# Kernel tuning notes

Hardware: AMD Instinct MI355X
Metric: run time of the kernel (lower is better)

Reference implementation:

```python
import math
import jax
import jax.numpy as jnp
import numpy as np
from jax import lax

B_, L, D_MODEL = 2, 1024, 2048
D_STATE, D_CONV, EXPAND = 16, 4, 2
D_INNER = EXPAND * D_MODEL          # 4096
DT_RANK = math.ceil(D_MODEL / 16)   # 128


def setup_inputs() -> dict:
    key = jax.random.key(0)
    ks = jax.random.split(key, 8)
    hidden_states = jax.random.normal(ks[0], (B_, L, D_MODEL), jnp.float32)
    in_proj_w = jax.random.normal(ks[1], (2 * D_INNER, D_MODEL), jnp.float32) * (D_MODEL ** -0.5)
    conv_w = jax.random.normal(ks[2], (D_INNER, D_CONV), jnp.float32) * (D_CONV ** -0.5)
    conv_b = jnp.zeros((D_INNER,), jnp.float32)
    x_proj_w = jax.random.normal(ks[3], (DT_RANK + 2 * D_STATE, D_INNER), jnp.float32) * (D_INNER ** -0.5)
    dt_std = DT_RANK ** -0.5
    dt_proj_w = jax.random.uniform(ks[4], (D_INNER, DT_RANK), jnp.float32, minval=-dt_std, maxval=dt_std)
    # dt bias init: softplus^{-1} of dt sampled log-uniform in [1e-3, 1e-1]
    dt = jnp.exp(jax.random.uniform(ks[5], (D_INNER,), jnp.float32)
                 * (math.log(0.1) - math.log(0.001)) + math.log(0.001))
    dt = jnp.clip(dt, 1e-4)
    dt_proj_b = dt + jnp.log(-jnp.expm1(-dt))
    A_log = jnp.log(jnp.broadcast_to(jnp.arange(1, D_STATE + 1, dtype=jnp.float32), (D_INNER, D_STATE)))
    D = jnp.ones((D_INNER,), jnp.float32)
    out_proj_w = jax.random.normal(ks[6], (D_MODEL, D_INNER), jnp.float32) * (D_INNER ** -0.5)
    return {
        'hidden_states': hidden_states, 'in_proj_w': in_proj_w,
        'conv_w': conv_w, 'conv_b': conv_b, 'x_proj_w': x_proj_w,
        'dt_proj_w': dt_proj_w, 'dt_proj_b': dt_proj_b,
        'A_log': A_log, 'D': D, 'out_proj_w': out_proj_w,
    }


def _silu(v):
    return v * jax.nn.sigmoid(v)


def _mamba_forward(hidden_states, in_proj_w, conv_w, conv_b, x_proj_w,
                   dt_proj_w, dt_proj_b, A_log, D, out_proj_w):
    b, l, _ = hidden_states.shape
    # in_proj: (b,l,d_model) -> (b, 2*d_inner, l)
    xz = jnp.einsum('bld,ed->bel', hidden_states, in_proj_w)
    x, z = xz[:, :D_INNER, :], xz[:, D_INNER:, :]
    A = -jnp.exp(A_log.astype(jnp.float32))  # (d_inner, d_state)
    # causal depthwise conv1d + SiLU
    xp = jnp.pad(x, ((0, 0), (0, 0), (D_CONV - 1, 0)))
    x = lax.conv_general_dilated(
        xp, conv_w[:, None, :], window_strides=(1,), padding='VALID',
        dimension_numbers=('NCH', 'OIH', 'NCH'), feature_group_count=D_INNER)
    x = _silu(x + conv_b[None, :, None])  # (b, d_inner, l)
    # x_proj -> dt, B, C
    x_dbl = jnp.einsum('bdl,kd->blk', x, x_proj_w)  # (b,l,dt_rank+2n)
    dt_lo = x_dbl[..., :DT_RANK]
    Bmat = x_dbl[..., DT_RANK:DT_RANK + D_STATE]          # (b,l,n)
    Cmat = x_dbl[..., DT_RANK + D_STATE:]                 # (b,l,n)
    delta = jax.nn.softplus(jnp.einsum('blr,dr->bld', dt_lo, dt_proj_w)
                            + dt_proj_b.astype(jnp.float32))  # (b,l,d)
    xt = jnp.transpose(x, (2, 0, 1))       # (l,b,d)
    dl = jnp.transpose(delta, (1, 0, 2))   # (l,b,d)
    Bl = jnp.transpose(Bmat, (1, 0, 2))    # (l,b,n)
    Cl = jnp.transpose(Cmat, (1, 0, 2))    # (l,b,n)

    def step(h, inp):
        d_t, B_t, C_t, x_t = inp
        dA = jnp.exp(d_t[..., None] * A)                       # (b,d,n)
        h = h * dA + d_t[..., None] * B_t[:, None, :] * x_t[..., None]
        y_t = jnp.sum(h * C_t[:, None, :], axis=-1)            # (b,d)
        return h, y_t

    h0 = jnp.zeros((b, D_INNER, D_STATE), jnp.float32)
    _, ys = lax.scan(step, h0, (dl, Bl, Cl, xt))  # ys: (l,b,d)
    y = jnp.transpose(ys, (1, 0, 2))              # (b,l,d)
    y = y + jnp.transpose(x, (0, 2, 1)) * D[None, None, :]
    y = y * _silu(jnp.transpose(z, (0, 2, 1)))
    out = jnp.einsum('bld,ed->ble', y, out_proj_w)  # (b,l,d_model)
    return out


def reference(hidden_states, in_proj_w, conv_w, conv_b, x_proj_w,
              dt_proj_w, dt_proj_b, A_log, D, out_proj_w):
    return _mamba_forward(hidden_states, in_proj_w, conv_w, conv_b, x_proj_w,
                          dt_proj_w, dt_proj_b, A_log, D, out_proj_w)
```

## Files before the change

kernel.cpp:

```cpp
#include <hip/hip_runtime.h>
#include <hip/hip_bf16.h>
#include <stdint.h>

#define BB 2
#define LL 1024
#define DMODEL 2048
#define DINNER 4096
#define DSTATE 16
#define DTRANK 128
#define XDBL_LD 256
#define CHUNK 64
#define NCH (LL / CHUNK)

typedef unsigned short ushort;
using short8 = __attribute__((ext_vector_type(8))) short;
using f32x4  = __attribute__((ext_vector_type(4))) float;
using us4    = __attribute__((ext_vector_type(4))) ushort;

__device__ __forceinline__ float bf2f(ushort u) {
    union { uint32_t i; float f; } v; v.i = ((uint32_t)u) << 16; return v.f;
}
__device__ __forceinline__ ushort f2bf(float f) {
    union { float f; uint32_t i; } v; v.f = f;
    uint32_t lsb = (v.i >> 16) & 1u;
    uint32_t r = v.i + 0x7FFFu + lsb;
    return (ushort)(r >> 16);
}

__device__ __forceinline__ void glds16(const ushort* g, ushort* l) {
    __builtin_amdgcn_global_load_lds(
        (const __attribute__((address_space(1))) void*)g,
        (__attribute__((address_space(3))) void*)l,
        16, 0, 0);
}

__global__ __launch_bounds__(256) void cvt_all(
    const float4* __restrict__ hidden, const float4* __restrict__ inproj,
    const float4* __restrict__ dtw, const float4* __restrict__ outp,
    const float4* __restrict__ xproj,
    us4* __restrict__ hid_h, us4* __restrict__ inp_h, us4* __restrict__ dtp_h,
    us4* __restrict__ outp_h, us4* __restrict__ xpp)
{
    long i = (long)blockIdx.x * 256 + threadIdx.x;
    const float4* src; us4* dst; long j;
    if (i < 1048576)      { src = hidden; dst = hid_h;  j = i; }
    else if (i < 5242880) { src = inproj; dst = inp_h;  j = i - 1048576; }
    else if (i < 5373952) { src = dtw;    dst = dtp_h;  j = i - 5242880; }
    else if (i < 7471104) { src = outp;   dst = outp_h; j = i - 5373952; }
    else {
        j = i - 7471104; dst = xpp;
        if (j >= 163840) { us4 z = {0, 0, 0, 0}; dst[j] = z; return; }
        src = xproj;
    }
    float4 v = src[j];
    us4 o; o.x = f2bf(v.x); o.y = f2bf(v.y); o.z = f2bf(v.z); o.w = f2bf(v.w);
    dst[j] = o;
}

template <bool WF, bool WH>
__global__ __launch_bounds__(512, 4) void gemm_bk32(
    const ushort* __restrict__ A, int lda,
    const ushort* __restrict__ Bm, int ldb,
    float* __restrict__ Cf, ushort* __restrict__ Ch, int ldc,
    int K)
{
    __shared__ __align__(16) ushort sA[2][128 * 32];
    __shared__ __align__(16) ushort sB[2][256 * 32];

    const int tid  = threadIdx.x;
    const int lane = tid & 63;
    const int wave = tid >> 6;
    const int wr   = wave >> 2;
    const int wcol = wave & 3;
    const int lrow = lane & 15;
    const int lg   = lane >> 4;
    const int kswz = (lg ^ ((lrow >> 1) & 3)) << 4;

    const int NT = gridDim.x, MT = gridDim.y;
    int mt, nt;
    if ((NT & 7) == 0) {
        int lin   = blockIdx.y * NT + blockIdx.x;
        int strip = NT >> 3;
        int xcd   = lin & 7;
        int idx   = lin >> 3;
        nt = xcd * strip + (idx % strip);
        mt = idx / strip;
    } else { mt = blockIdx.y; nt = blockIdx.x; }
    const long m0 = (long)mt * 128;
    const long n0 = (long)nt * 256;

    const long zoff = (long)blockIdx.z;
    A  += zoff * (long)K;
    Bm += zoff * (long)K;
    const long Mrows = (long)MT * 128;
    if (WF) Cf += zoff * Mrows * (long)ldc;

    f32x4 acc[4][4] = {};

    const int srow = tid >> 2;
    const int scol = (((tid & 3) ^ ((tid >> 3) & 3)) << 3);
    const ushort* Ag = A  + (m0 + srow) * (long)lda + scol;
    const ushort* Bg = Bm + (n0 + srow) * (long)ldb + scol;
    const long bstep = 128 * (long)ldb;

    const int NKT = K >> 5;

    glds16(Ag, &sA[0][0] + tid * 8);
    glds16(Bg, &sB[0][0] + tid * 8);
    glds16(Bg + bstep, &sB[0][0] + (512 + tid) * 8);
    __syncthreads();

    const int arow0 = (wr * 64 + lrow) * 64 + kswz;
    const int brow0 = (wcol * 64 + lrow) * 64 + kswz;

    for (int kt = 0; kt < NKT; ++kt) {
        const int p = kt & 1;
        const char* sap = (const char*)&sA[p][0];
        const char* sbp = (const char*)&sB[p][0];
        ushort* dA = &sA[p ^ 1][0] + tid * 8;
        ushort* dB = &sB[p ^ 1][0] + tid * 8;
        const long kn = (long)(kt + 1) << 5;
        const bool pf = (kt + 1 < NKT);

        short8 af[4], bf[4];
        #pragma unroll
        for (int i = 0; i < 4; ++i)
            af[i] = *(const short8*)(sap + arow0 + (i * 16) * 64);
        #pragma unroll
        for (int j = 0; j < 4; ++j)
            bf[j] = *(const short8*)(sbp + brow0 + (j * 16) * 64);

        if (pf) {
            glds16(Ag + kn, dA);
            glds16(Bg + kn, dB);
            glds16(Bg + bstep + kn, dB + 512 * 8);
        }

        __builtin_amdgcn_s_setprio(1);
        #pragma unroll
        for (int i = 0; i < 4; ++i)
            #pragma unroll
            for (int j = 0; j < 4; ++j)
                acc[i][j] = __builtin_amdgcn_mfma_f32_16x16x32_bf16(
                    af[i], bf[j], acc[i][j], 0, 0, 0);
        __builtin_amdgcn_s_setprio(0);

        __syncthreads();
    }

    const int r0 = (lane >> 4) * 4;
    const int c0 = lane & 15;
    #pragma unroll
    for (int i = 0; i < 4; ++i) {
        #pragma unroll
        for (int j = 0; j < 4; ++j) {
            const long col = n0 + wcol * 64 + j * 16 + c0;
            #pragma unroll
            for (int r = 0; r < 4; ++r) {
                const long row = m0 + wr * 64 + i * 16 + r0 + r;
                const float v = acc[i][j][r];
                const long idx = row * (long)ldc + col;
                if (WF) Cf[idx] = v;
                if (WH) Ch[idx] = f2bf(v);
            }
        }
    }
}

template <bool WF, bool WH>
__global__ __launch_bounds__(512, 2) void gemm_nt256(
    const ushort* __restrict__ A, int lda,
    const ushort* __restrict__ Bm, int ldb,
    float* __restrict__ Cf, ushort* __restrict__ Ch, int ldc,
    int K)
{
    __shared__ __align__(16) ushort sA[2][256 * 64];
    __shared__ __align__(16) ushort sB[2][256 * 64];

    const int tid  = threadIdx.x;
    const int lane = tid & 63;
    const int wave = tid >> 6;
    const int wr   = wave >> 2;
    const int wcol = wave & 3;
    const int lrow = lane & 15;
    const int lg   = lane >> 4;
    const int s7   = lane & 7;
    const int kb0 = ((0 + lg) ^ s7) << 4;
    const int kb1 = ((4 + lg) ^ s7) << 4;

    const int NT = gridDim.x, MT = gridDim.y;
    int mt, nt;
    if ((NT & 7) == 0) {
        int lin   = blockIdx.y * NT + blockIdx.x;
        int strip = NT >> 3;
        int xcd   = lin & 7;
        int idx   = lin >> 3;
        nt = xcd * strip + (idx % strip);
        mt = idx / strip;
    } else { mt = blockIdx.y; nt = blockIdx.x; }
    const long m0 = (long)mt * 256;
    const long n0 = (long)nt * 256;

    const long zoff = (long)blockIdx.z;
    A  += zoff * (long)K;
    Bm += zoff * (long)K;
    const long Mrows = (long)MT * 256;
    if (WF) Cf += zoff * Mrows * (long)ldc;

    f32x4 acc[8][4] = {};

    const int sr   = tid >> 3;
    const int scol = (((tid & 7) ^ (sr & 7)) << 3);
    const ushort* Ag = A  + (m0 + sr) * (long)lda + scol;
    const ushort* Bg = Bm + (n0 + sr) * (long)ldb + scol;

    const int NKT = K >> 6;

    {
        ushort* dA0 = &sA[0][0] + tid * 8;
        ushort* dB0 = &sB[0][0] + tid * 8;
        #pragma unroll
        for (int c = 0; c < 4; ++c) {
            glds16(Ag + (c * 64) * (long)lda, dA0 + c * 4096);
            glds16(Bg + (c * 64) * (long)ldb, dB0 + c * 4096);
        }
    }
    __syncthreads();

    const int arow0 = (wr * 128 + lrow) * 128;
    const int brow0 = (wcol * 64 + lrow) * 128;

    for (int kt = 0; kt < NKT; ++kt) {
        const int p = kt & 1;
        const char* sap = (const char*)&sA[p][0];
        const char* sbp = (const char*)&sB[p][0];
        ushort* dA = &sA[p ^ 1][0] + tid * 8;
        ushort* dB = &sB[p ^ 1][0] + tid * 8;
        const long kn = (long)(kt + 1) << 6;
        const bool pf = (kt + 1 < NKT);

        short8 bf[4][2];
        #pragma unroll
        for (int j = 0; j < 4; ++j) {
            const int bb = brow0 + (j * 16) * 128;
            bf[j][0] = *(const short8*)(sbp + bb + kb0);
            bf[j][1] = *(const short8*)(sbp + bb + kb1);
        }

        #pragma unroll
        for (int mh = 0; mh < 2; ++mh) {
            short8 af[4][2];
            #pragma unroll
            for (int i4 = 0; i4 < 4; ++i4) {
                const int ab = arow0 + (mh * 64 + i4 * 16) * 128;
                af[i4][0] = *(const short8*)(sap + ab + kb0);
                af[i4][1] = *(const short8*)(sap + ab + kb1);
            }
            if (pf) {
                if (mh == 0) {
                    #pragma unroll
                    for (int c = 0; c < 4; ++c)
                        glds16(Ag + (c * 64) * (long)lda + kn, dA + c * 4096);
                } else {
                    #pragma unroll
                    for (int c = 0; c < 4; ++c)
                        glds16(Bg + (c * 64) * (long)ldb + kn, dB + c * 4096);
                }
            }
            __builtin_amdgcn_s_setprio(1);
            #pragma unroll
            for (int ks = 0; ks < 2; ++ks)
                #pragma unroll
                for (int i4 = 0; i4 < 4; ++i4)
                    #pragma unroll
                    for (int j = 0; j < 4; ++j)
                        acc[mh * 4 + i4][j] =
                            __builtin_amdgcn_mfma_f32_16x16x32_bf16(
                                af[i4][ks], bf[j][ks],
                                acc[mh * 4 + i4][j], 0, 0, 0);
            __builtin_amdgcn_s_setprio(0);
        }
        __syncthreads();
    }

    const int r0 = (lane >> 4) * 4;
    const int c0 = lane & 15;
    #pragma unroll
    for (int i = 0; i < 8; ++i) {
        #pragma unroll
        for (int j = 0; j < 4; ++j) {
            const long col = n0 + wcol * 64 + j * 16 + c0;
            #pragma unroll
            for (int r = 0; r < 4; ++r) {
                const long row = m0 + wr * 128 + i * 16 + r0 + r;
                const float v = acc[i][j][r];
                const long idx = row * (long)ldc + col;
                if (WF) Cf[idx] = v;
                if (WH) Ch[idx] = f2bf(v);
            }
        }
    }
}

template <int EPI, bool WF, bool WH>
__global__ __launch_bounds__(256) void gemm_nt(
    const ushort* __restrict__ A, int lda,
    const ushort* __restrict__ Bm, int ldb,
    float* __restrict__ Cf, ushort* __restrict__ Ch, int ldc,
    int K, const float* __restrict__ bias)
{
    __shared__ __align__(16) ushort sA[128 * 64];
    __shared__ __align__(16) ushort sB[128 * 64];

    const int tid  = threadIdx.x;
    const int lane = tid & 63;
    const int wave = tid >> 6;
    const int wr = wave >> 1, wc = wave & 1;

    const int NT = gridDim.x, MT = gridDim.y;
    int mt, nt;
    if ((NT & 7) == 0) {
        int lin   = blockIdx.y * NT + blockIdx.x;
        int strip = NT >> 3;
        int xcd   = lin & 7;
        int idx   = lin >> 3;
        nt = xcd * strip + (idx % strip);
        mt = idx / strip;
    } else { mt = blockIdx.y; nt = blockIdx.x; }
    const long m0 = (long)mt * 128;
    const long n0 = (long)nt * 128;

    const long zoff = (long)blockIdx.z;
    A  += zoff * (long)K;
    Bm += zoff * (long)K;
    const long Mrows = (long)MT * 128;
    if (WF) Cf += zoff * Mrows * (long)ldc;
    if (WH) Ch += zoff * Mrows * (long)ldc;

    f32x4 acc[4][4] = {};

    const int lrow = lane & 15;
    const int lko  = (lane >> 4) << 3;

    const int sr = tid >> 3;
    const int sc = (tid & 7) << 3;
    const ushort* Ag = A  + (m0 + sr) * (long)lda + sc;
    const ushort* Bg = Bm + (n0 + sr) * (long)ldb + sc;
    ushort* lA = sA + tid * 8;
    ushort* lB = sB + tid * 8;

    for (int k0 = 0; k0 < K; k0 += 64) {
        __syncthreads();
        #pragma unroll
        for (int c = 0; c < 4; ++c) {
            glds16(Ag + (c * 32) * (long)lda + k0, lA + c * 2048);
            glds16(Bg + (c * 32) * (long)ldb + k0, lB + c * 2048);
        }
        __syncthreads();

        #pragma unroll
        for (int ks = 0; ks < 2; ++ks) {
            short8 af[4], bf[4];
            #pragma unroll
            for (int i = 0; i < 4; ++i)
                af[i] = *(const short8*)&sA[(wr * 64 + i * 16 + lrow) * 64 + ks * 32 + lko];
            #pragma unroll
            for (int j = 0; j < 4; ++j)
                bf[j] = *(const short8*)&sB[(wc * 64 + j * 16 + lrow) * 64 + ks * 32 + lko];

            #pragma unroll
            for (int i = 0; i < 4; ++i)
                #pragma unroll
                for (int j = 0; j < 4; ++j)
                    acc[i][j] = __builtin_amdgcn_mfma_f32_16x16x32_bf16(
                        af[i], bf[j], acc[i][j], 0, 0, 0);
        }
    }

    const int r0 = (lane >> 4) * 4;
    const int c0 = lane & 15;
    #pragma unroll
    for (int i = 0; i < 4; ++i) {
        #pragma unroll
        for (int j = 0; j < 4; ++j) {
            long col = n0 + wc * 64 + j * 16 + c0;
            float bv = 0.f;
            if (EPI == 1) bv = bias[col];
            #pragma unroll
            for (int r = 0; r < 4; ++r) {
                long row = m0 + wr * 64 + i * 16 + r0 + r;
                float v = acc[i][j][r];
                if (EPI == 1) {
                    v += bv;
                    v = (v > 20.f) ? v : log1pf(__expf(v));
                }
                long idx = row * (long)ldc + col;
                if (WF) Cf[idx] = v;
                if (WH) Ch[idx] = f2bf(v);
            }
        }
    }
}

template <int NZ, bool WH_>
__global__ __launch_bounds__(256) void reduce_k(
    const float4* __restrict__ parts, long stride4, int n4,
    float4* __restrict__ outF, us4* __restrict__ outH)
{
    int i = blockIdx.x * 256 + threadIdx.x;
    if (i >= n4) return;
    float4 s = parts[i];
    #pragma unroll
    for (int z = 1; z < NZ; ++z) {
        float4 v = parts[(long)z * stride4 + i];
        s.x += v.x; s.y += v.y; s.z += v.z; s.w += v.w;
    }
    if (outF) outF[i] = s;
    if (WH_) {
        us4 o; o.x = f2bf(s.x); o.y = f2bf(s.y); o.z = f2bf(s.z); o.w = f2bf(s.w);
        outH[i] = o;
    }
}

__global__ __launch_bounds__(256) void conv_silu_kernel(
    const ushort* __restrict__ xz,
    const float* __restrict__ cw,
    const float* __restrict__ cb,
    ushort* __restrict__ xc)
{
    int gid = blockIdx.x * 256 + threadIdx.x;
    int d  = gid & (DINNER - 1);
    int rl = gid >> 12;
    int l  = rl & (LL - 1);
    float acc = cb[d];
    #pragma unroll
    for (int j = 0; j < 4; ++j) {
        int li = l - 3 + j;
        if (li >= 0)
            acc += cw[d * 4 + j] * bf2f(xz[(long)(rl - 3 + j) * 8192 + d]);
    }
    float s = acc / (1.f + __expf(-acc));
    xc[gid] = f2bf(s);
}

__global__ __launch_bounds__(256) void scan_p1(
    const ushort* __restrict__ delta,
    const ushort* __restrict__ xc,
    const float*  __restrict__ xdbl,
    const float*  __restrict__ A_log,
    float* __restrict__ Hbuf,
    float* __restrict__ sumdt_buf)
{
    __shared__ float sB[CHUNK * 16];
    const int tid = threadIdx.x;
    const int k = blockIdx.y, b = blockIdx.z;
    const int d = blockIdx.x * 256 + tid;
    const int row0 = b * LL + k * CHUNK;

    #pragma unroll
    for (int i = 0; i < 4; ++i) {
        int idx = i * 256 + tid;
        sB[idx] = xdbl[(long)(row0 + (idx >> 4)) * XDBL_LD + DTRANK + (idx & 15)];
    }
    __syncthreads();

    float A[DSTATE];
    const float4* Ap = (const float4*)(A_log + d * DSTATE);
    #pragma unroll
    for (int i = 0; i < 4; ++i) {
        float4 v = Ap[i];
        A[i*4+0] = -__expf(v.x); A[i*4+1] = -__expf(v.y);
        A[i*4+2] = -__expf(v.z); A[i*4+3] = -__expf(v.w);
    }

    float H[DSTATE];
    #pragma unroll
    for (int s = 0; s < DSTATE; ++s) H[s] = 0.f;
    float sumdt = 0.f;

    for (int t = 0; t < CHUNK; ++t) {
        const long row = row0 + t;
        const float dt = bf2f(delta[row * DINNER + d]);
        const float xv = bf2f(xc[row * DINNER + d]);
        const float dx = dt * xv;
        sumdt += dt;
        #pragma unroll
        for (int s = 0; s < DSTATE; ++s) {
            float dA = __expf(dt * A[s]);
            H[s] = H[s] * dA + dx * sB[t * 16 + s];
        }
    }

    const long o = ((long)(b * NCH + k) * DINNER + d) * DSTATE;
    float4* Ho = (float4*)(Hbuf + o);
    #pragma unroll
    for (int i = 0; i < 4; ++i) {
        float4 v; v.x = H[i*4+0]; v.y = H[i*4+1]; v.z = H[i*4+2]; v.w = H[i*4+3];
        Ho[i] = v;
    }
    sumdt_buf[(b * NCH + k) * DINNER + d] = sumdt;
}

__global__ __launch_bounds__(256) void scan_p2(
    const float* __restrict__ A_log,
    const float* __restrict__ sumdt_buf,
    float* __restrict__ Hbuf)
{
    int gid = blockIdx.x * 256 + threadIdx.x;
    int b = gid >> 16;
    int rem = gid & 65535;
    int d = rem >> 4, s = rem & 15;
    float A = -__expf(A_log[d * DSTATE + s]);
    float h = 0.f;
    for (int k = 0; k < NCH; ++k) {
        long idx = ((long)(b * NCH + k) * DINNER + d) * DSTATE + s;
        float Hk = Hbuf[idx];
        float sd = sumdt_buf[(b * NCH + k) * DINNER + d];
        Hbuf[idx] = h;
        h = h * __expf(A * sd) + Hk;
    }
}

__global__ __launch_bounds__(256) void scan_p3(
    const ushort* __restrict__ delta,
    const ushort* __restrict__ xc,
    const float*  __restrict__ xdbl,
    const ushort* __restrict__ xz,
    const float*  __restrict__ A_log,
    const float*  __restrict__ Dp,
    const float*  __restrict__ hin,
    ushort* __restrict__ y)
{
    __shared__ float sBC[CHUNK * 32];
    const int tid = threadIdx.x;
    const int k = blockIdx.y, b = blockIdx.z;
    const int d = blockIdx.x * 256 + tid;
    const int row0 = b * LL + k * CHUNK;

    #pragma unroll
    for (int i = 0; i < 8; ++i) {
        int idx = i * 256 + tid;
        sBC[idx] = xdbl[(long)(row0 + (idx >> 5)) * XDBL_LD + DTRANK + (idx & 31)];
    }
    __syncthreads();

    float A[DSTATE];
    const float4* Ap = (const float4*)(A_log + d * DSTATE);
    #pragma unroll
    for (int i = 0; i < 4; ++i) {
        float4 v = Ap[i];
        A[i*4+0] = -__expf(v.x); A[i*4+1] = -__expf(v.y);
        A[i*4+2] = -__expf(v.z); A[i*4+3] = -__expf(v.w);
    }
    const float Dd = Dp[d];

    float h[DSTATE];
    const float4* Hp = (const float4*)(hin + ((long)(b * NCH + k) * DINNER + d) * DSTATE);
    #pragma unroll
    for (int i = 0; i < 4; ++i) {
        float4 v = Hp[i];
        h[i*4+0] = v.x; h[i*4+1] = v.y; h[i*4+2] = v.z; h[i*4+3] = v.w;
    }

    for (int t = 0; t < CHUNK; ++t) {
        const long row = row0 + t;
        const float dt = bf2f(delta[row * DINNER + d]);
        const float xv = bf2f(xc[row * DINNER + d]);
        const float dx = dt * xv;
        float yt = 0.f;
        #pragma unroll
        for (int s = 0; s < DSTATE; ++s) {
            float dA = __expf(dt * A[s]);
            h[s] = h[s] * dA + dx * sBC[t * 32 + s];
            yt += h[s] * sBC[t * 32 + 16 + s];
        }
        yt += xv * Dd;
        const float zv = bf2f(xz[row * 8192 + DINNER + d]);
        yt *= zv / (1.f + __expf(-zv));
        y[row * DINNER + d] = f2bf(yt);
    }
}

extern "C" void kernel_launch(void* const* d_in, const int* in_sizes, int n_in,
                              void* d_out, int out_size, void* d_ws, size_t ws_size,
                              hipStream_t stream)
{
    const float* hidden    = (const float*)d_in[0];
    const float* in_proj   = (const float*)d_in[1];
    const float* conv_w    = (const float*)d_in[2];
    const float* conv_b    = (const float*)d_in[3];
    const float* x_proj    = (const float*)d_in[4];
    const float* dt_proj_w = (const float*)d_in[5];
    const float* dt_proj_b = (const float*)d_in[6];
    const float* A_log     = (const float*)d_in[7];
    const float* Dp        = (const float*)d_in[8];
    const float* out_proj  = (const float*)d_in[9];
    float* out = (float*)d_out;

    char* ws = (char*)d_ws;
    ushort* xz_h    = (ushort*)(ws);
    ushort* xc      = (ushort*)(ws + 33554432);
    ushort* xpp     = (ushort*)(ws + 50331648);
    float*  xdbl    = (float*)(ws + 52428800);
    ushort* xdblh   = (ushort*)(ws + 54525952);
    ushort* delta_h = (ushort*)(ws + 55574528);
    ushort* yb      = (ushort*)(ws + 72351744);
    ushort* hid_h   = (ushort*)(ws + 89128960);
    ushort* inp_h   = (ushort*)(ws + 97517568);
    float*  parts   = (float*)(ws + 97517568);
    float*  Hbuf    = (float*)(ws + 97517568);
    float*  sumdt   = (float*)(ws + 105906176);
    ushort* dtp_h   = (ushort*)(ws + 131072000);
    ushort* outp_h  = (ushort*)(ws + 132120576);
    float*  parts2  = (float*)(ws);

    const int M = BB * LL;

    cvt_all<<<30208, 256, 0, stream>>>(
        (const float4*)hidden, (const float4*)in_proj, (const float4*)dt_proj_w,
        (const float4*)out_proj, (const float4*)x_proj,
        (us4*)hid_h, (us4*)inp_h, (us4*)dtp_h, (us4*)outp_h, (us4*)xpp);

    gemm_bk32<false, true><<<dim3(8192 / 256, M / 128), 512, 0, stream>>>(
        hid_h, DMODEL, inp_h, DMODEL, nullptr, xz_h, 8192, DMODEL);

    conv_silu_kernel<<<(M * DINNER) / 256, 256, 0, stream>>>(xz_h, conv_w, conv_b, xc);

    gemm_nt<0, true, false><<<dim3(XDBL_LD / 128, M / 128, 16), 256, 0, stream>>>(
        xc, DINNER, xpp, DINNER, parts, nullptr, XDBL_LD, DINNER / 16, nullptr);
    reduce_k<16, true><<<(M * XDBL_LD / 4 + 255) / 256, 256, 0, stream>>>(
        (const float4*)parts, (long)M * XDBL_LD / 4, M * XDBL_LD / 4,
        (float4*)xdbl, (us4*)xdblh);

    gemm_nt<1, false, true><<<dim3(DINNER / 128, M / 128), 256, 0, stream>>>(
        xdblh, XDBL_LD, dtp_h, DTRANK, nullptr, delta_h, DINNER, DTRANK, dt_proj_b);

    scan_p1<<<dim3(DINNER / 256, NCH, BB), 256, 0, stream>>>(
        delta_h, xc, xdbl, A_log, Hbuf, sumdt);
    scan_p2<<<(BB * DINNER * DSTATE) / 256, 256, 0, stream>>>(
        A_log, sumdt, Hbuf);
    scan_p3<<<dim3(DINNER / 256, NCH, BB), 256, 0, stream>>>(
        delta_h, xc, xdbl, xz_h, A_log, Dp, Hbuf, yb);

    gemm_nt256<true, false><<<dim3(DMODEL / 256, M / 256, 4), 512, 0, stream>>>(
        yb, DINNER, outp_h, DINNER, parts2, nullptr, DMODEL, DINNER / 4);
    reduce_k<4, false><<<(M * DMODEL / 4 + 255) / 256, 256, 0, stream>>>(
        (const float4*)parts2, (long)M * DMODEL / 4, M * DMODEL / 4,
        (float4*)out, nullptr);
}
```

Before: 461.8 us.

## Swap in_proj to 256x256 GEMM and drop split-K for out_proj

The in_proj GEMM moves from the 128x256 BK=32 kernel to the existing 256x256 BK=64 kernel, which reuses each loaded operand across more output. The out_proj GEMM drops its 4-way split-K plus separate reduction in favour of a new 128x128 BK=64 double-buffered kernel that writes fp32 output directly. This removes the partial-sum write, the re-read and one kernel launch. In exchange, out_proj runs 256 blocks over the full K of 4096, which may under-fill the GPU, and the larger in_proj tiles give fewer blocks.

```diff
diff --git a/kernel.cpp b/kernel.cpp
--- a/kernel.cpp
+++ b/kernel.cpp
@@ -55,116 +55,6 @@
     float4 v = src[j];
     us4 o; o.x = f2bf(v.x); o.y = f2bf(v.y); o.z = f2bf(v.z); o.w = f2bf(v.w);
     dst[j] = o;
-}
-
-template <bool WF, bool WH>
-__global__ __launch_bounds__(512, 4) void gemm_bk32(
-    const ushort* __restrict__ A, int lda,
-    const ushort* __restrict__ Bm, int ldb,
-    float* __restrict__ Cf, ushort* __restrict__ Ch, int ldc,
-    int K)
-{
-    __shared__ __align__(16) ushort sA[2][128 * 32];
-    __shared__ __align__(16) ushort sB[2][256 * 32];
-
-    const int tid  = threadIdx.x;
-    const int lane = tid & 63;
-    const int wave = tid >> 6;
-    const int wr   = wave >> 2;
-    const int wcol = wave & 3;
-    const int lrow = lane & 15;
-    const int lg   = lane >> 4;
-    const int kswz = (lg ^ ((lrow >> 1) & 3)) << 4;
-
-    const int NT = gridDim.x, MT = gridDim.y;
-    int mt, nt;
-    if ((NT & 7) == 0) {
-        int lin   = blockIdx.y * NT + blockIdx.x;
-        int strip = NT >> 3;
-        int xcd   = lin & 7;
-        int idx   = lin >> 3;
-        nt = xcd * strip + (idx % strip);
-        mt = idx / strip;
-    } else { mt = blockIdx.y; nt = blockIdx.x; }
-    const long m0 = (long)mt * 128;
-    const long n0 = (long)nt * 256;
-
-    const long zoff = (long)blockIdx.z;
-    A  += zoff * (long)K;
-    Bm += zoff * (long)K;
-    const long Mrows = (long)MT * 128;
-    if (WF) Cf += zoff * Mrows * (long)ldc;
-
-    f32x4 acc[4][4] = {};
-
-    const int srow = tid >> 2;
-    const int scol = (((tid & 3) ^ ((tid >> 3) & 3)) << 3);
-    const ushort* Ag = A  + (m0 + srow) * (long)lda + scol;
-    const ushort* Bg = Bm + (n0 + srow) * (long)ldb + scol;
-    const long bstep = 128 * (long)ldb;
-
-    const int NKT = K >> 5;
-
-    glds16(Ag, &sA[0][0] + tid * 8);
-    glds16(Bg, &sB[0][0] + tid * 8);
-    glds16(Bg + bstep, &sB[0][0] + (512 + tid) * 8);
-    __syncthreads();
-
-    const int arow0 = (wr * 64 + lrow) * 64 + kswz;
-    const int brow0 = (wcol * 64 + lrow) * 64 + kswz;
-
-    for (int kt = 0; kt < NKT; ++kt) {
-        const int p = kt & 1;
-        const char* sap = (const char*)&sA[p][0];
-        const char* sbp = (const char*)&sB[p][0];
-        ushort* dA = &sA[p ^ 1][0] + tid * 8;
-        ushort* dB = &sB[p ^ 1][0] + tid * 8;
-        const long kn = (long)(kt + 1) << 5;
-        const bool pf = (kt + 1 < NKT);
-
-        short8 af[4], bf[4];
-        #pragma unroll
-        for (int i = 0; i < 4; ++i)
-            af[i] = *(const short8*)(sap + arow0 + (i * 16) * 64);
-        #pragma unroll
-        for (int j = 0; j < 4; ++j)
-            bf[j] = *(const short8*)(sbp + brow0 + (j * 16) * 64);
-
-        if (pf) {
-            glds16(Ag + kn, dA);
-            glds16(Bg + kn, dB);
-            glds16(Bg + bstep + kn, dB + 512 * 8);
-        }
-
-        __builtin_amdgcn_s_setprio(1);
-        #pragma unroll
-        for (int i = 0; i < 4; ++i)
-            #pragma unroll
-            for (int j = 0; j < 4; ++j)
-                acc[i][j] = __builtin_amdgcn_mfma_f32_16x16x32_bf16(
-                    af[i], bf[j], acc[i][j], 0, 0, 0);
-        __builtin_amdgcn_s_setprio(0);
-
-        __syncthreads();
-    }
-
-    const int r0 = (lane >> 4) * 4;
-    const int c0 = lane & 15;
-    #pragma unroll
-    for (int i = 0; i < 4; ++i) {
-        #pragma unroll
-        for (int j = 0; j < 4; ++j) {
-            const long col = n0 + wcol * 64 + j * 16 + c0;
-            #pragma unroll
-            for (int r = 0; r < 4; ++r) {
-                const long row = m0 + wr * 64 + i * 16 + r0 + r;
-                const float v = acc[i][j][r];
-                const long idx = row * (long)ldc + col;
-                if (WF) Cf[idx] = v;
-                if (WH) Ch[idx] = f2bf(v);
-            }
-        }
-    }
 }
 
 template <bool WF, bool WH>
@@ -302,6 +192,127 @@
     }
 }
 
+template <bool WF, bool WH>
+__global__ __launch_bounds__(256, 2) void gemm_nt128d(
+    const ushort* __restrict__ A, int lda,
+    const ushort* __restrict__ Bm, int ldb,
+    float* __restrict__ Cf, ushort* __restrict__ Ch, int ldc,
+    int K)
+{
+    __shared__ __align__(16) ushort sA[2][128 * 64];
+    __shared__ __align__(16) ushort sB[2][128 * 64];
+
+    const int tid  = threadIdx.x;
+    const int lane = tid & 63;
+    const int wave = tid >> 6;
+    const int wr   = wave >> 1;
+    const int wc   = wave & 1;
+    const int lrow = lane & 15;
+    const int lg   = lane >> 4;
+    const int s7   = lane & 7;
+    const int kb0 = ((0 + lg) ^ s7) << 4;
+    const int kb1 = ((4 + lg) ^ s7) << 4;
+
+    const int NT = gridDim.x, MT = gridDim.y;
+    int mt, nt;
+    if ((NT & 7) == 0) {
+        int lin   = blockIdx.y * NT + blockIdx.x;
+        int strip = NT >> 3;
+        int xcd   = lin & 7;
+        int idx   = lin >> 3;
+        nt = xcd * strip + (idx % strip);
+        mt = idx / strip;
+    } else { mt = blockIdx.y; nt = blockIdx.x; }
+    const long m0 = (long)mt * 128;
+    const long n0 = (long)nt * 128;
+
+    f32x4 acc[4][4] = {};
+
+    const int sr   = tid >> 3;
+    const int scol = (((tid & 7) ^ (sr & 7)) << 3);
+    const ushort* Ag = A  + (m0 + sr) * (long)lda + scol;
+    const ushort* Bg = Bm + (n0 + sr) * (long)ldb + scol;
+
+    const int NKT = K >> 6;
+
+    {
+        ushort* dA0 = &sA[0][0] + tid * 8;
+        ushort* dB0 = &sB[0][0] + tid * 8;
+        #pragma unroll
+        for (int c = 0; c < 4; ++c) {
+            glds16(Ag + (c * 32) * (long)lda, dA0 + c * 2048);
+            glds16(Bg + (c * 32) * (long)ldb, dB0 + c * 2048);
+        }
+    }
+    __syncthreads();
+
+    const int arow0 = (wr * 64 + lrow) * 128;
+    const int brow0 = (wc * 64 + lrow) * 128;
+
+    for (int kt = 0; kt < NKT; ++kt) {
+        const int p = kt & 1;
+        const char* sap = (const char*)&sA[p][0];
+        const char* sbp = (const char*)&sB[p][0];
+        ushort* dA = &sA[p ^ 1][0] + tid * 8;
+        ushort* dB = &sB[p ^ 1][0] + tid * 8;
+        const long kn = (long)(kt + 1) << 6;
+        const bool pf = (kt + 1 < NKT);
+
+        short8 af[4][2], bf[4][2];
+        #pragma unroll
+        for (int i = 0; i < 4; ++i) {
+            const int ab = arow0 + (i * 16) * 128;
+            af[i][0] = *(const short8*)(sap + ab + kb0);
+            af[i][1] = *(const short8*)(sap + ab + kb1);
+        }
+        #pragma unroll
+        for (int j = 0; j < 4; ++j) {
+            const int bb = brow0 + (j * 16) * 128;
+            bf[j][0] = *(const short8*)(sbp + bb + kb0);
+            bf[j][1] = *(const short8*)(sbp + bb + kb1);
+        }
+
+        if (pf) {
+            #pragma unroll
+            for (int c = 0; c < 4; ++c) {
+                glds16(Ag + (c * 32) * (long)lda + kn, dA + c * 2048);
+                glds16(Bg + (c * 32) * (long)ldb + kn, dB + c * 2048);
+            }
+        }
+
+        __builtin_amdgcn_s_setprio(1);
+        #pragma unroll
+        for (int ks = 0; ks < 2; ++ks)
+            #pragma unroll
+            for (int i = 0; i < 4; ++i)
+                #pragma unroll
+                for (int j = 0; j < 4; ++j)
+                    acc[i][j] = __builtin_amdgcn_mfma_f32_16x16x32_bf16(
+                        af[i][ks], bf[j][ks], acc[i][j], 0, 0, 0);
+        __builtin_amdgcn_s_setprio(0);
+
+        __syncthreads();
+    }
+
+    const int r0 = (lane >> 4) * 4;
+    const int c0 = lane & 15;
+    #pragma unroll
+    for (int i = 0; i < 4; ++i) {
+        #pragma unroll
+        for (int j = 0; j < 4; ++j) {
+            const long col = n0 + wc * 64 + j * 16 + c0;
+            #pragma unroll
+            for (int r = 0; r < 4; ++r) {
+                const long row = m0 + wr * 64 + i * 16 + r0 + r;
+                const float v = acc[i][j][r];
+                const long idx = row * (long)ldc + col;
+                if (WF) Cf[idx] = v;
+                if (WH) Ch[idx] = f2bf(v);
+            }
+        }
+    }
+}
+
 template <int EPI, bool WF, bool WH>
 __global__ __launch_bounds__(256) void gemm_nt(
     const ushort* __restrict__ A, int lda,
@@ -612,7 +623,6 @@
     float*  sumdt   = (float*)(ws + 105906176);
     ushort* dtp_h   = (ushort*)(ws + 131072000);
     ushort* outp_h  = (ushort*)(ws + 132120576);
-    float*  parts2  = (float*)(ws);
 
     const int M = BB * LL;
 
@@ -621,7 +631,7 @@
         (const float4*)out_proj, (const float4*)x_proj,
         (us4*)hid_h, (us4*)inp_h, (us4*)dtp_h, (us4*)outp_h, (us4*)xpp);
 
-    gemm_bk32<false, true><<<dim3(8192 / 256, M / 128), 512, 0, stream>>>(
+    gemm_nt256<false, true><<<dim3(8192 / 256, M / 256), 512, 0, stream>>>(
         hid_h, DMODEL, inp_h, DMODEL, nullptr, xz_h, 8192, DMODEL);
 
     conv_silu_kernel<<<(M * DINNER) / 256, 256, 0, stream>>>(xz_h, conv_w, conv_b, xc);
@@ -642,9 +652,6 @@
     scan_p3<<<dim3(DINNER / 256, NCH, BB), 256, 0, stream>>>(
         delta_h, xc, xdbl, xz_h, A_log, Dp, Hbuf, yb);
 
-    gemm_nt256<true, false><<<dim3(DMODEL / 256, M / 256, 4), 512, 0, stream>>>(
-        yb, DINNER, outp_h, DINNER, parts2, nullptr, DMODEL, DINNER / 4);
-    reduce_k<4, false><<<(M * DMODEL / 4 + 255) / 256, 256, 0, stream>>>(
-        (const float4*)parts2, (long)M * DMODEL / 4, M * DMODEL / 4,
-        (float4*)out, nullptr);
-}
+    gemm_nt128d<true, false><<<dim3(DMODEL / 128, M / 128), 256, 0, stream>>>(
+        yb, DINNER, outp_h, DINNER, out, nullptr, DMODEL, DINNER);
+}
```

New measurement: 509.3 us. 10.3% more time.
